# Kernel tuning notes

Measured on AMD Instinct MI355X. Metric: run time of the kernel, lower is better.

The kernel has to match this reference:

```python
import jax, jax.numpy as jnp
import numpy as np

HEADS, DIM_HEAD, LANDMARKS, PINV_ITERS = 8, 64, 256, 6
DIM, SIZE, N_CLASSES, N_PATCH = 512, 1024, 2, 16384
LN_EPS = 1e-5


def layer_norm(x, g, b):
    mu = x.mean(-1, keepdims=True)
    var = ((x - mu) ** 2).mean(-1, keepdims=True)
    return (x - mu) / jnp.sqrt(var + LN_EPS) * g + b


def moore_penrose_pinv(x, iters):
    # x: [b, h, m, m]; global max over all batch/head entries (matches torch.max)
    abs_x = jnp.abs(x)
    col = abs_x.sum(-1).max()
    row = abs_x.sum(-2).max()
    z = jnp.swapaxes(x, -1, -2) / (col * row)
    I = jnp.eye(x.shape[-1], dtype=x.dtype)
    for _ in range(iters):
        xz = x @ z
        z = 0.25 * z @ (13 * I - xz @ (15 * I - xz @ (7 * I - xz)))
    return z


def nystrom_attention(x, qkv_w, out_w, out_b, res_w):
    b, n, _ = x.shape
    m = LANDMARKS
    pad = (m - n % m) % m
    xp = jnp.pad(x, ((0, 0), (pad, 0), (0, 0)))  # pad at FRONT of sequence
    npad = n + pad
    qkv = xp @ qkv_w  # [b, npad, 3*h*d]
    q, k, v = jnp.split(qkv, 3, axis=-1)
    to_h = lambda t: t.reshape(b, npad, HEADS, DIM_HEAD).transpose(0, 2, 1, 3)
    q, k, v = to_h(q), to_h(k), to_h(v)
    q = q * (DIM_HEAD ** -0.5)
    l = npad // m  # tokens per landmark segment
    q_l = q.reshape(b, HEADS, m, l, DIM_HEAD).sum(3) / l
    k_l = k.reshape(b, HEADS, m, l, DIM_HEAD).sum(3) / l
    sim1 = jnp.einsum('bhid,bhjd->bhij', q, k_l)     # [b,h,npad,m]
    sim2 = jnp.einsum('bhid,bhjd->bhij', q_l, k_l)   # [b,h,m,m]
    sim3 = jnp.einsum('bhid,bhjd->bhij', q_l, k)     # [b,h,m,npad]
    a1 = jax.nn.softmax(sim1, -1)
    a2 = jax.nn.softmax(sim2, -1)
    a3 = jax.nn.softmax(sim3, -1)
    out = (a1 @ moore_penrose_pinv(a2, PINV_ITERS)) @ (a3 @ v)
    # residual depthwise conv over sequence dim, kernel (33,1), groups=heads
    res = jax.lax.conv_general_dilated(
        v, res_w, (1, 1), [(16, 16), (0, 0)],
        dimension_numbers=('NCHW', 'OIHW', 'NCHW'), feature_group_count=HEADS)
    out = out + res
    out = out.transpose(0, 2, 1, 3).reshape(b, npad, HEADS * DIM_HEAD)
    out = out @ out_w + out_b
    return out[:, -n:]


def trans_layer(x, ng, nb, qkv_w, out_w, out_b, res_w):
    return x + nystrom_attention(layer_norm(x, ng, nb), qkv_w, out_w, out_b, res_w)


def ppeg(x, w7, b7, w5, b5, w3, b3, H, W):
    cls_tok, feat = x[:, :1], x[:, 1:]
    B, N, C = feat.shape
    f = feat.transpose(0, 2, 1).reshape(B, C, H, W)
    def dw(w, b, p):
        y = jax.lax.conv_general_dilated(
            f, w, (1, 1), [(p, p), (p, p)],
            dimension_numbers=('NCHW', 'OIHW', 'NCHW'), feature_group_count=C)
        return y + b[None, :, None, None]
    out = dw(w7, b7, 3) + f + dw(w5, b5, 2) + dw(w3, b3, 1)
    out = out.reshape(B, C, H * W).transpose(0, 2, 1)
    return jnp.concatenate([cls_tok, out], axis=1)


def setup_inputs() -> dict:
    key = jax.random.key(0)
    ks = jax.random.split(key, 24)
    rn = lambda k, s, sc=0.02: jax.random.normal(k, s, jnp.float32) * sc
    inner = HEADS * DIM_HEAD  # 512
    return {
        'data': jax.random.normal(ks[0], (1, N_PATCH, SIZE), jnp.float32),
        'fc1_w': rn(ks[1], (SIZE, DIM)), 'fc1_b': jnp.zeros((DIM,), jnp.float32),
        'cls_token': jax.random.normal(ks[2], (1, 1, DIM), jnp.float32),
        'l1_ng': jnp.ones((DIM,), jnp.float32), 'l1_nb': jnp.zeros((DIM,), jnp.float32),
        'l1_qkv': rn(ks[3], (DIM, 3 * inner)),
        'l1_ow': rn(ks[4], (inner, DIM)), 'l1_ob': jnp.zeros((DIM,), jnp.float32),
        'l1_rw': rn(ks[5], (HEADS, 1, 33, 1)),
        'l2_ng': jnp.ones((DIM,), jnp.float32), 'l2_nb': jnp.zeros((DIM,), jnp.float32),
        'l2_qkv': rn(ks[6], (DIM, 3 * inner)),
        'l2_ow': rn(ks[7], (inner, DIM)), 'l2_ob': jnp.zeros((DIM,), jnp.float32),
        'l2_rw': rn(ks[8], (HEADS, 1, 33, 1)),
        'p_w7': rn(ks[9], (DIM, 1, 7, 7)), 'p_b7': jnp.zeros((DIM,), jnp.float32),
        'p_w5': rn(ks[10], (DIM, 1, 5, 5)), 'p_b5': jnp.zeros((DIM,), jnp.float32),
        'p_w3': rn(ks[11], (DIM, 1, 3, 3)), 'p_b3': jnp.zeros((DIM,), jnp.float32),
        'n_g': jnp.ones((DIM,), jnp.float32), 'n_b': jnp.zeros((DIM,), jnp.float32),
        'fc2_w': rn(ks[12], (DIM, N_CLASSES)), 'fc2_b': jnp.zeros((N_CLASSES,), jnp.float32),
    }


def reference(data, fc1_w, fc1_b, cls_token, l1_ng, l1_nb, l1_qkv, l1_ow, l1_ob, l1_rw,
              l2_ng, l2_nb, l2_qkv, l2_ow, l2_ob, l2_rw,
              p_w7, p_b7, p_w5, p_b5, p_w3, p_b3, n_g, n_b, fc2_w, fc2_b):
    h = jax.nn.relu(data @ fc1_w + fc1_b)  # [B, N, 512]
    B, N = h.shape[0], h.shape[1]
    _H = _W = int(np.ceil(np.sqrt(N)))
    add_length = _H * _W - N
    h = jnp.concatenate([h, h[:, :add_length, :]], axis=1)
    cls = jnp.broadcast_to(cls_token, (B, 1, h.shape[2]))
    h = jnp.concatenate([cls, h], axis=1)
    h = trans_layer(h, l1_ng, l1_nb, l1_qkv, l1_ow, l1_ob, l1_rw)
    h = ppeg(h, p_w7, p_b7, p_w5, p_b5, p_w3, p_b3, _H, _W)
    h = trans_layer(h, l2_ng, l2_nb, l2_qkv, l2_ow, l2_ob, l2_rw)
    h = layer_norm(h, n_g, n_b)[:, 0]
    logits = h @ fc2_w + fc2_b
    y_hat = jnp.argmax(logits, axis=1)
    y_prob = jax.nn.softmax(logits, axis=1)
    return (logits, y_prob, y_hat)
```

## Files before the change

### kernel.cpp

```cpp
#include <hip/hip_runtime.h>
#include <hip/hip_bf16.h>


#define NT 16385
#define NP 16640
#define PADR 255
#define DIMF 512
#define QKVW 1536
#define NHEAD 8
#define DH 64
#define NLM 256
#define LSEG 65
#define A3V_TC 20

typedef short bf16x8 __attribute__((ext_vector_type(8)));
typedef short bf16x4 __attribute__((ext_vector_type(4)));
typedef float f32x4 __attribute__((ext_vector_type(4)));

__device__ __forceinline__ void gload_lds16(const void* g, void* l) {
    __builtin_amdgcn_global_load_lds(
        (const __attribute__((address_space(1))) void*)g,
        (__attribute__((address_space(3))) void*)l, 16, 0, 0);
}

__device__ __forceinline__ float2 b2f(const __hip_bfloat16* p) {
    ushort2 u = *(const ushort2*)p;
    float2 r;
    r.x = __uint_as_float((unsigned)u.x << 16);
    r.y = __uint_as_float((unsigned)u.y << 16);
    return r;
}

__device__ __forceinline__ unsigned f2b16(float a, float b) {
    union { unsigned u; __hip_bfloat16 h[2]; } c;
    c.h[0] = __float2bfloat16(a); c.h[1] = __float2bfloat16(b);
    return c.u;
}

__device__ __forceinline__ bf16x4 f4b(float a, float b, float c, float d) {
    union { bf16x4 v; __hip_bfloat16 h[4]; } u;
    u.h[0] = __float2bfloat16(a); u.h[1] = __float2bfloat16(b);
    u.h[2] = __float2bfloat16(c); u.h[3] = __float2bfloat16(d);
    return u.v;
}

__global__ __launch_bounds__(256) void gemm_bf16_k(
    const __hip_bfloat16* __restrict__ A, const __hip_bfloat16* __restrict__ BT,
    const float* __restrict__ bias, const float* __restrict__ Cacc,
    float* __restrict__ C, __hip_bfloat16* __restrict__ C16,
    int M, int N, int K, int MA, int relu)
{
    __shared__ __align__(16) __hip_bfloat16 Asl[128 * 64];
    __shared__ __align__(16) __hip_bfloat16 Bsl[128 * 64];
    int tid = threadIdx.x;
    int wid = tid >> 6, lane = tid & 63;
    int m0 = blockIdx.y << 7, n0 = blockIdx.x << 7;
    int wr = (wid >> 1) << 6, wc = (wid & 1) << 6;
    f32x4 acc[4][4] = {};
    int lr = lane >> 3, lk = (lane & 7) << 3;
    for (int kt = 0; kt < K; kt += 64) {
#pragma unroll
        for (int i = 0; i < 4; ++i) {
            int ch = wid * 4 + i;
            int rowA = m0 + ch * 8 + lr;
            rowA = rowA < MA ? rowA : (MA - 1);
            gload_lds16(A + (size_t)rowA * K + kt + lk, &Asl[ch * 512]);
            int rowB = n0 + ch * 8 + lr;
            gload_lds16(BT + (size_t)rowB * K + kt + lk, &Bsl[ch * 512]);
        }
        __syncthreads();
#pragma unroll
        for (int ks = 0; ks < 2; ++ks) {
            int kb = ks * 32 + (lane >> 4) * 8;
            bf16x8 af[4], bfr[4];
#pragma unroll
            for (int m = 0; m < 4; ++m)
                af[m] = *(const bf16x8*)&Asl[(wr + m * 16 + (lane & 15)) * 64 + kb];
#pragma unroll
            for (int n = 0; n < 4; ++n)
                bfr[n] = *(const bf16x8*)&Bsl[(wc + n * 16 + (lane & 15)) * 64 + kb];
#pragma unroll
            for (int m = 0; m < 4; ++m)
#pragma unroll
                for (int n = 0; n < 4; ++n)
                    acc[m][n] = __builtin_amdgcn_mfma_f32_16x16x32_bf16(
                        af[m], bfr[n], acc[m][n], 0, 0, 0);
        }
        __syncthreads();
    }
    int cr = (lane >> 4) << 2, cc = lane & 15;
#pragma unroll
    for (int m = 0; m < 4; ++m) {
#pragma unroll
        for (int i = 0; i < 4; ++i) {
            int gm = m0 + wr + m * 16 + cr + i;
            if (gm >= M) continue;
#pragma unroll
            for (int n = 0; n < 4; ++n) {
                int gn = n0 + wc + n * 16 + cc;
                float v = acc[m][n][i];
                if (bias) v += bias[gn];
                if (Cacc) v += Cacc[(size_t)gm * N + gn];
                if (relu) v = fmaxf(v, 0.f);
                if (C16) C16[(size_t)gm * N + gn] = __float2bfloat16(v);
                else C[(size_t)gm * N + gn] = v;
            }
        }
    }
}

__global__ __launch_bounds__(256) void transcvt_k(const float* __restrict__ W,
    __hip_bfloat16* __restrict__ WT, int K, int N)
{
    __shared__ float t[32][33];
    int nt = N >> 5;
    int n0 = (blockIdx.x % nt) << 5, k0 = (blockIdx.x / nt) << 5;
    int tx = threadIdx.x & 31, ty = threadIdx.x >> 5;
    for (int r = ty; r < 32; r += 8) t[r][tx] = W[(size_t)(k0 + r) * N + n0 + tx];
    __syncthreads();
    for (int r = ty; r < 32; r += 8)
        WT[(size_t)(n0 + r) * K + k0 + tx] = __float2bfloat16(t[tx][r]);
}

__global__ __launch_bounds__(256) void cvt_k(const float4* __restrict__ in,
    ushort4* __restrict__ out, int n4)
{
    int i = blockIdx.x * 256 + threadIdx.x;
    if (i >= n4) return;
    float4 v = in[i];
    union { __hip_bfloat16 h[4]; ushort4 u; } cv;
    cv.h[0] = __float2bfloat16(v.x); cv.h[1] = __float2bfloat16(v.y);
    cv.h[2] = __float2bfloat16(v.z); cv.h[3] = __float2bfloat16(v.w);
    out[i] = cv.u;
}

__global__ __launch_bounds__(256) void vtrans_k(const __hip_bfloat16* __restrict__ qkvb16,
    __hip_bfloat16* __restrict__ vT16)
{
    int h = blockIdx.y;
    int t0 = blockIdx.x << 6;
    __shared__ float tile[64][65];
    int tid = threadIdx.x;
    for (int e = tid; e < 512; e += 256) {
        int r = e >> 3, c8 = (e & 7) << 3;
        union { bf16x8 v; __hip_bfloat16 hh[8]; } u;
        u.v = *(const bf16x8*)(qkvb16 + (size_t)(t0 + r) * QKVW + 1024 + (h << 6) + c8);
#pragma unroll
        for (int j = 0; j < 8; ++j) tile[r][c8 + j] = __bfloat162float(u.hh[j]);
    }
    __syncthreads();
    for (int e = tid; e < 512; e += 256) {
        int d = e >> 3, t8 = (e & 7) << 3;
        union { bf16x8 v; __hip_bfloat16 hh[8]; } u;
#pragma unroll
        for (int j = 0; j < 8; ++j) u.hh[j] = __float2bfloat16(tile[t8 + j][d]);
        *(bf16x8*)(vT16 + ((size_t)(h << 6) + d) * NP + t0 + t8) = u.v;
    }
}

__global__ __launch_bounds__(64) void ln_k(const float* __restrict__ in,
    const float* __restrict__ g, const float* __restrict__ b,
    __hip_bfloat16* __restrict__ out, int rows)
{
    int r = blockIdx.x;
    if (r >= rows) return;
    int lane = threadIdx.x;
    const float* xr = in + (size_t)r * DIMF;
    float v[8], s = 0.f;
#pragma unroll
    for (int i = 0; i < 8; ++i) { v[i] = xr[i * 64 + lane]; s += v[i]; }
#pragma unroll
    for (int off = 32; off; off >>= 1) s += __shfl_xor(s, off);
    float mu = s * (1.f / 512.f);
    float vs = 0.f;
#pragma unroll
    for (int i = 0; i < 8; ++i) { float d = v[i] - mu; vs += d * d; }
#pragma unroll
    for (int off = 32; off; off >>= 1) vs += __shfl_xor(vs, off);
    float rstd = rsqrtf(vs * (1.f / 512.f) + 1e-5f);
    __hip_bfloat16* orow = out + (size_t)r * DIMF;
#pragma unroll
    for (int i = 0; i < 8; ++i) {
        int d = i * 64 + lane;
        orow[d] = __float2bfloat16((v[i] - mu) * rstd * g[d] + b[d]);
    }
}

__global__ __launch_bounds__(256) void landmark_k(const __hip_bfloat16* __restrict__ qkvb16,
    float* __restrict__ ql, float* __restrict__ kl,
    __hip_bfloat16* __restrict__ ql16, __hip_bfloat16* __restrict__ kl16)
{
    int bx = blockIdx.x;
    int h = bx >> 8, j = bx & 255;
    int w = threadIdx.x >> 6, d = threadIdx.x & 63;
    __shared__ float pq[4][64], pk[4][64];
    float qs = 0.f, ks = 0.f;
    for (int u = w; u < LSEG; u += 4) {
        size_t addr = (size_t)(j * LSEG + u) * QKVW + (h << 6) + d;
        qs += __bfloat162float(qkvb16[addr]);
        ks += __bfloat162float(qkvb16[addr + 512]);
    }
    pq[w][d] = qs; pk[w][d] = ks;
    __syncthreads();
    if (threadIdx.x < 64) {
        float q = pq[0][d] + pq[1][d] + pq[2][d] + pq[3][d];
        float k = pk[0][d] + pk[1][d] + pk[2][d] + pk[3][d];
        float qm = q * (1.f / 65.f) * 0.125f;
        float km = k * (1.f / 65.f);
        ql[(size_t)bx * 64 + d] = qm;
        kl[(size_t)bx * 64 + d] = km;
        ql16[(size_t)bx * 64 + d] = __float2bfloat16(qm);
        kl16[(size_t)bx * 64 + d] = __float2bfloat16(km);
    }
}

__global__ __launch_bounds__(256) void a2_k(const float* __restrict__ ql,
    const float* __restrict__ kl, float* __restrict__ a2, __hip_bfloat16* __restrict__ a2_16)
{
    int h = blockIdx.x >> 8, i = blockIdx.x & 255;
    int j = threadIdx.x;
    __shared__ float qs[64];
    __shared__ float red[256];
    if (j < 64) qs[j] = ql[((size_t)(h << 8) + i) * 64 + j];
    __syncthreads();
    const float* kr = kl + ((size_t)(h << 8) + j) * 64;
    float s = 0.f;
#pragma unroll 8
    for (int d = 0; d < 64; ++d) s += qs[d] * kr[d];
    red[j] = s; __syncthreads();
    for (int st = 128; st; st >>= 1) { if (j < st) red[j] = fmaxf(red[j], red[j + st]); __syncthreads(); }
    float mx = red[0]; __syncthreads();
    float p = __expf(s - mx);
    red[j] = p; __syncthreads();
    for (int st = 128; st; st >>= 1) { if (j < st) red[j] += red[j + st]; __syncthreads(); }
    float v = p / red[0];
    a2[((size_t)h << 16) + i * 256 + j] = v;
    a2_16[((size_t)h << 16) + i * 256 + j] = __float2bfloat16(v);
}

__global__ __launch_bounds__(256) void zinit_k(const float* __restrict__ a2,
    __hip_bfloat16* __restrict__ zr16, __hip_bfloat16* __restrict__ zT16)
{
    int h = blockIdx.x, t = threadIdx.x;
    const float* X = a2 + ((size_t)h << 16);
    __shared__ float red[256];
    __shared__ float tl[64][65];
    float rs = 0.f;
    const float4* Xr = (const float4*)(X + (size_t)t * 256);
    for (int j = 0; j < 64; ++j) {
        float4 v = Xr[j];
        rs += fabsf(v.x) + fabsf(v.y) + fabsf(v.z) + fabsf(v.w);
    }
    red[t] = rs; __syncthreads();
    for (int st = 128; st; st >>= 1) { if (t < st) red[t] = fmaxf(red[t], red[t + st]); __syncthreads(); }
    float colv = red[0]; __syncthreads();
    float cs = 0.f;
    for (int i = 0; i < 256; ++i) cs += fabsf(X[i * 256 + t]);
    red[t] = cs; __syncthreads();
    for (int st = 128; st; st >>= 1) { if (t < st) red[t] = fmaxf(red[t], red[t + st]); __syncthreads(); }
    float rowv = red[0];
    float inv = 1.f / (colv * rowv);
    int cl = t & 63, rg = t >> 6;
    for (int tr = 0; tr < 4; ++tr)
        for (int tc = 0; tc < 4; ++tc) {
            __syncthreads();
#pragma unroll
            for (int k = 0; k < 16; ++k) {
                int rl = (k << 2) + rg;
                tl[rl][cl] = X[(size_t)(tr * 64 + rl) * 256 + tc * 64 + cl];
            }
            __syncthreads();
#pragma unroll
            for (int k = 0; k < 16; ++k) {
                int rl = (k << 2) + rg;
                zT16[((size_t)h << 16) + (size_t)(tr * 64 + rl) * 256 + tc * 64 + cl] =
                    __float2bfloat16(tl[rl][cl] * inv);
                zr16[((size_t)h << 16) + (size_t)(tc * 64 + rl) * 256 + tr * 64 + cl] =
                    __float2bfloat16(tl[cl][rl] * inv);
            }
        }
}

__global__ __launch_bounds__(256) void pgemm1_k(
    const __hip_bfloat16* __restrict__ a2_16, const __hip_bfloat16* __restrict__ zT16,
    __hip_bfloat16* __restrict__ xz16, __hip_bfloat16* __restrict__ t1T16)
{
    int h = blockIdx.y, n0 = blockIdx.x << 6;
    int lane = threadIdx.x & 63;
    int r0 = (threadIdx.x >> 6) << 6;
    int rA = lane & 15, g = lane >> 4, kp = g << 3;
    const __hip_bfloat16* Ah = a2_16 + ((size_t)h << 16);
    const __hip_bfloat16* Bh = zT16 + ((size_t)h << 16);
    f32x4 acc[4][4] = {};
    for (int ks = 0; ks < 8; ++ks) {
        bf16x8 af[4], bfr[4];
#pragma unroll
        for (int m = 0; m < 4; ++m)
            af[m] = *(const bf16x8*)&Ah[(size_t)(r0 + m * 16 + rA) * 256 + ks * 32 + kp];
#pragma unroll
        for (int n = 0; n < 4; ++n)
            bfr[n] = *(const bf16x8*)&Bh[(size_t)(n0 + n * 16 + rA) * 256 + ks * 32 + kp];
#pragma unroll
        for (int m = 0; m < 4; ++m)
#pragma unroll
            for (int n = 0; n < 4; ++n)
                acc[m][n] = __builtin_amdgcn_mfma_f32_16x16x32_bf16(af[m], bfr[n], acc[m][n], 0, 0, 0);
    }
    __hip_bfloat16* xzh = xz16 + ((size_t)h << 16);
    __hip_bfloat16* t1h = t1T16 + ((size_t)h << 16);
#pragma unroll
    for (int m = 0; m < 4; ++m)
#pragma unroll
        for (int i = 0; i < 4; ++i) {
            int gr = r0 + m * 16 + (g << 2) + i;
#pragma unroll
            for (int n = 0; n < 4; ++n) {
                int gc = n0 + n * 16 + rA;
                float v = acc[m][n][i];
                xzh[(size_t)gr * 256 + gc] = __float2bfloat16(v);
                t1h[(size_t)gc * 256 + gr] = __float2bfloat16((gr == gc ? 7.f : 0.f) - v);
            }
        }
}

__global__ __launch_bounds__(256) void pgemm3_k(
    const __hip_bfloat16* __restrict__ xz16, const __hip_bfloat16* __restrict__ t1T16,
    const __hip_bfloat16* __restrict__ zr16,
    __hip_bfloat16* __restrict__ znr16, __hip_bfloat16* __restrict__ znT16)
{
    __shared__ __align__(16) __hip_bfloat16 tA[64][264];
    __shared__ __align__(16) __hip_bfloat16 tB[64][264];
    int h = blockIdx.y, n0 = blockIdx.x << 6;
    int lane = threadIdx.x & 63;
    int r0 = (threadIdx.x >> 6) << 6;
    int rA = lane & 15, g = lane >> 4, kp = g << 3;
    const __hip_bfloat16* Xh = xz16 + ((size_t)h << 16);
    const __hip_bfloat16* T1h = t1T16 + ((size_t)h << 16);
    {
        f32x4 acc[4][4] = {};
        for (int ks = 0; ks < 8; ++ks) {
            bf16x8 af[4], bfr[4];
#pragma unroll
            for (int m = 0; m < 4; ++m)
                af[m] = *(const bf16x8*)&Xh[(size_t)(r0 + m * 16 + rA) * 256 + ks * 32 + kp];
#pragma unroll
            for (int n = 0; n < 4; ++n)
                bfr[n] = *(const bf16x8*)&T1h[(size_t)(n0 + n * 16 + rA) * 256 + ks * 32 + kp];
#pragma unroll
            for (int m = 0; m < 4; ++m)
#pragma unroll
                for (int n = 0; n < 4; ++n)
                    acc[m][n] = __builtin_amdgcn_mfma_f32_16x16x32_bf16(af[m], bfr[n], acc[m][n], 0, 0, 0);
        }
#pragma unroll
        for (int m = 0; m < 4; ++m)
#pragma unroll
            for (int n = 0; n < 4; ++n) {
                int gr0 = r0 + m * 16 + (g << 2);
                int cl = n * 16 + rA;
                *(bf16x4*)&tA[cl][gr0] = f4b(
                    ((gr0 + 0 == n0 + cl) ? 15.f : 0.f) - acc[m][n][0],
                    ((gr0 + 1 == n0 + cl) ? 15.f : 0.f) - acc[m][n][1],
                    ((gr0 + 2 == n0 + cl) ? 15.f : 0.f) - acc[m][n][2],
                    ((gr0 + 3 == n0 + cl) ? 15.f : 0.f) - acc[m][n][3]);
            }
    }
    __syncthreads();
    {
        f32x4 acc[4][4] = {};
        for (int ks = 0; ks < 8; ++ks) {
            bf16x8 af[4], bfr[4];
#pragma unroll
            for (int m = 0; m < 4; ++m)
                af[m] = *(const bf16x8*)&Xh[(size_t)(r0 + m * 16 + rA) * 256 + ks * 32 + kp];
#pragma unroll
            for (int n = 0; n < 4; ++n)
                bfr[n] = *(const bf16x8*)&tA[n * 16 + rA][ks * 32 + kp];
#pragma unroll
            for (int m = 0; m < 4; ++m)
#pragma unroll
                for (int n = 0; n < 4; ++n)
                    acc[m][n] = __builtin_amdgcn_mfma_f32_16x16x32_bf16(af[m], bfr[n], acc[m][n], 0, 0, 0);
        }
#pragma unroll
        for (int m = 0; m < 4; ++m)
#pragma unroll
            for (int n = 0; n < 4; ++n) {
                int gr0 = r0 + m * 16 + (g << 2);
                int cl = n * 16 + rA;
                *(bf16x4*)&tB[cl][gr0] = f4b(
                    ((gr0 + 0 == n0 + cl) ? 13.f : 0.f) - acc[m][n][0],
                    ((gr0 + 1 == n0 + cl) ? 13.f : 0.f) - acc[m][n][1],
                    ((gr0 + 2 == n0 + cl) ? 13.f : 0.f) - acc[m][n][2],
                    ((gr0 + 3 == n0 + cl) ? 13.f : 0.f) - acc[m][n][3]);
            }
    }
    __syncthreads();
    {
        const __hip_bfloat16* Zh = zr16 + ((size_t)h << 16);
        f32x4 acc[4][4] = {};
        for (int ks = 0; ks < 8; ++ks) {
            bf16x8 af[4], bfr[4];
#pragma unroll
            for (int m = 0; m < 4; ++m)
                af[m] = *(const bf16x8*)&Zh[(size_t)(r0 + m * 16 + rA) * 256 + ks * 32 + kp];
#pragma unroll
            for (int n = 0; n < 4; ++n)
                bfr[n] = *(const bf16x8*)&tB[n * 16 + rA][ks * 32 + kp];
#pragma unroll
            for (int m = 0; m < 4; ++m)
#pragma unroll
                for (int n = 0; n < 4; ++n)
                    acc[m][n] = __builtin_amdgcn_mfma_f32_16x16x32_bf16(af[m], bfr[n], acc[m][n], 0, 0, 0);
        }
        __hip_bfloat16* zrh = znr16 + ((size_t)h << 16);
        __hip_bfloat16* zth = znT16 + ((size_t)h << 16);
#pragma unroll
        for (int m = 0; m < 4; ++m)
#pragma unroll
            for (int i = 0; i < 4; ++i) {
                int gr = r0 + m * 16 + (g << 2) + i;
#pragma unroll
                for (int n = 0; n < 4; ++n) {
                    int gc = n0 + n * 16 + rA;
                    float v = 0.25f * acc[m][n][i];
                    zrh[(size_t)gr * 256 + gc] = __float2bfloat16(v);
                    zth[(size_t)gc * 256 + gr] = __float2bfloat16(v);
                }
            }
    }
}

__global__ __launch_bounds__(256) void wm_k(
    const __hip_bfloat16* __restrict__ zr16, const __hip_bfloat16* __restrict__ a3vT16,
    __hip_bfloat16* __restrict__ wmT16)
{
    int h = blockIdx.x;
    int lane = threadIdx.x & 63;
    int r0 = (threadIdx.x >> 6) << 6;
    int rA = lane & 15, g = lane >> 4, kp = g << 3;
    const __hip_bfloat16* Zh = zr16 + ((size_t)h << 16);
    const __hip_bfloat16* Bh = a3vT16 + ((size_t)h << 14);
    f32x4 acc[4][4] = {};
    for (int ks = 0; ks < 8; ++ks) {
        bf16x8 af[4], bfr[4];
#pragma unroll
        for (int m = 0; m < 4; ++m)
            af[m] = *(const bf16x8*)&Zh[(size_t)(r0 + m * 16 + rA) * 256 + ks * 32 + kp];
#pragma unroll
        for (int n = 0; n < 4; ++n)
            bfr[n] = *(const bf16x8*)&Bh[(size_t)(n * 16 + rA) * 256 + ks * 32 + kp];
#pragma unroll
        for (int m = 0; m < 4; ++m)
#pragma unroll
            for (int n = 0; n < 4; ++n)
                acc[m][n] = __builtin_amdgcn_mfma_f32_16x16x32_bf16(af[m], bfr[n], acc[m][n], 0, 0, 0);
    }
    __hip_bfloat16* Wh = wmT16 + ((size_t)h << 14);
#pragma unroll
    for (int m = 0; m < 4; ++m)
#pragma unroll
        for (int i = 0; i < 4; ++i) {
            int gr = r0 + m * 16 + (g << 2) + i;
#pragma unroll
            for (int n = 0; n < 4; ++n)
                Wh[(size_t)(n * 16 + rA) * 256 + gr] = __float2bfloat16(acc[m][n][i]);
        }
}

__global__ __launch_bounds__(128) void a3v_flash_k(
    const __hip_bfloat16* __restrict__ ql16, const __hip_bfloat16* __restrict__ qkvb16,
    const __hip_bfloat16* __restrict__ vT16,
    float* __restrict__ opart, float* __restrict__ mpart, float* __restrict__ lpart)
{
    int bx = blockIdx.x;
    int h = bx >> 2, qb = bx & 3;
    int tc = blockIdx.y;
    int wv = threadIdx.x >> 6;
    int lane = threadIdx.x & 63;
    int rA = lane & 15, g = lane >> 4, kp = g << 3;
    __shared__ __align__(16) __hip_bfloat16 Plds[2][32 * 64];
    char* P = (char*)&Plds[wv][0];

    bf16x8 qa[2][2];
    const __hip_bfloat16* qlh = ql16 + ((size_t)h << 14);
#pragma unroll
    for (int m = 0; m < 2; ++m)
#pragma unroll
        for (int ks = 0; ks < 2; ++ks)
            qa[m][ks] = *(const bf16x8*)(qlh +
                (size_t)((qb << 6) + (wv << 5) + (m << 4) + rA) * 64 + ks * 32 + kp);

    const __hip_bfloat16* kg = qkvb16 + 512 + (h << 6);
    const __hip_bfloat16* vg = vT16 + ((size_t)(h << 6)) * NP;

    f32x4 O[2][4] = {};
    float m_[2][4], l_[2][4];
#pragma unroll
    for (int m = 0; m < 2; ++m)
#pragma unroll
        for (int i = 0; i < 4; ++i) { m_[m][i] = -3e38f; l_[m][i] = 0.f; }

    for (int tile = tc * 13; tile < tc * 13 + 13; ++tile) {
        int t0 = tile << 6;
        f32x4 S[2][4] = {};
#pragma unroll
        for (int n = 0; n < 4; ++n)
#pragma unroll
            for (int ks = 0; ks < 2; ++ks) {
                bf16x8 kb = *(const bf16x8*)(kg + (size_t)(t0 + (n << 4) + rA) * QKVW + ks * 32 + kp);
                S[0][n] = __builtin_amdgcn_mfma_f32_16x16x32_bf16(qa[0][ks], kb, S[0][n], 0, 0, 0);
                S[1][n] = __builtin_amdgcn_mfma_f32_16x16x32_bf16(qa[1][ks], kb, S[1][n], 0, 0, 0);
            }
        float f_[2][4];
#pragma unroll
        for (int m = 0; m < 2; ++m)
#pragma unroll
            for (int i = 0; i < 4; ++i) {
                float mx = fmaxf(fmaxf(S[m][0][i], S[m][1][i]), fmaxf(S[m][2][i], S[m][3][i]));
#pragma unroll
                for (int msk = 8; msk; msk >>= 1) mx = fmaxf(mx, __shfl_xor(mx, msk));
                float mn = fmaxf(m_[m][i], mx);
                float f = __expf(m_[m][i] - mn);
                int r = (m << 4) + (g << 2) + i;
                int swz = (r & 7) << 4;
                float sum = 0.f;
#pragma unroll
                for (int n = 0; n < 4; ++n) {
                    float p = __expf(S[m][n][i] - mn);
                    sum += p;
                    int byte = (r << 7) + (((n << 4) + rA) << 1);
                    *(__hip_bfloat16*)(P + (byte ^ swz)) = __float2bfloat16(p);
                }
#pragma unroll
                for (int msk = 8; msk; msk >>= 1) sum += __shfl_xor(sum, msk);
                l_[m][i] = l_[m][i] * f + sum;
                m_[m][i] = mn;
                f_[m][i] = f;
            }
#pragma unroll
        for (int m = 0; m < 2; ++m)
#pragma unroll
            for (int i = 0; i < 4; ++i) {
                float f = f_[m][i];
#pragma unroll
                for (int n = 0; n < 4; ++n) O[m][n][i] *= f;
            }
#pragma unroll
        for (int ks2 = 0; ks2 < 2; ++ks2) {
            bf16x8 pa[2];
#pragma unroll
            for (int m = 0; m < 2; ++m) {
                int rr = (m << 4) + rA;
                int byte = (rr << 7) + ((ks2 * 32 + kp) << 1);
                pa[m] = *(const bf16x8*)(P + (byte ^ ((rr & 7) << 4)));
            }
#pragma unroll
            for (int n = 0; n < 4; ++n) {
                bf16x8 vb = *(const bf16x8*)(vg + (size_t)((n << 4) + rA) * NP + t0 + ks2 * 32 + kp);
                O[0][n] = __builtin_amdgcn_mfma_f32_16x16x32_bf16(pa[0], vb, O[0][n], 0, 0, 0);
                O[1][n] = __builtin_amdgcn_mfma_f32_16x16x32_bf16(pa[1], vb, O[1][n], 0, 0, 0);
            }
        }
    }
    int pb2 = (bx << 1) | wv;
    size_t obase = ((size_t)pb2 * A3V_TC + tc) * 2048;
#pragma unroll
    for (int m = 0; m < 2; ++m)
#pragma unroll
        for (int i = 0; i < 4; ++i) {
            int r = (m << 4) + (g << 2) + i;
#pragma unroll
            for (int n = 0; n < 4; ++n)
                opart[obase + (size_t)r * 64 + (n << 4) + rA] = O[m][n][i];
            if (rA == 0) {
                mpart[((size_t)pb2 * A3V_TC + tc) * 32 + r] = m_[m][i];
                lpart[((size_t)pb2 * A3V_TC + tc) * 32 + r] = l_[m][i];
            }
        }
}

__global__ __launch_bounds__(64) void a3v_comb_k(const float* __restrict__ opart,
    const float* __restrict__ mpart, const float* __restrict__ lpart,
    __hip_bfloat16* __restrict__ a3vT16)
{
    int pb = blockIdx.x, d = threadIdx.x;
    int h = pb >> 3;
    for (int r = 0; r < 32; ++r) {
        float M = -3e38f;
        for (int tc = 0; tc < A3V_TC; ++tc)
            M = fmaxf(M, mpart[((size_t)pb * A3V_TC + tc) * 32 + r]);
        float L = 0.f, od = 0.f;
        for (int tc = 0; tc < A3V_TC; ++tc) {
            float w = __expf(mpart[((size_t)pb * A3V_TC + tc) * 32 + r] - M);
            L += lpart[((size_t)pb * A3V_TC + tc) * 32 + r] * w;
            od += w * opart[((size_t)pb * A3V_TC + tc) * 2048 + (size_t)r * 64 + d];
        }
        int j = ((pb & 7) << 5) + r;
        a3vT16[((size_t)((h << 6) + d) << 8) + j] = __float2bfloat16(od / L);
    }
}

__global__ __launch_bounds__(128) void attnout_mfma_k(
    const __hip_bfloat16* __restrict__ qkvb16, const __hip_bfloat16* __restrict__ kl16,
    const __hip_bfloat16* __restrict__ wmT16, float* __restrict__ o)
{
    int h = blockIdx.y;
    int rbase = (blockIdx.x << 6) + ((threadIdx.x >> 6) << 5);
    int lane = threadIdx.x & 63;
    int rA = lane & 15;
    int g = lane >> 4;
    int kp = g << 3;
    __shared__ __align__(16) __hip_bfloat16 Plds[2][32 * 256];
    char* P = (char*)&Plds[threadIdx.x >> 6][0];

    bf16x8 qa[2][2];
#pragma unroll
    for (int m = 0; m < 2; ++m)
#pragma unroll
        for (int ks = 0; ks < 2; ++ks)
            qa[m][ks] = *(const bf16x8*)(qkvb16 +
                (size_t)(rbase + m * 16 + rA) * QKVW + (h << 6) + ks * 32 + kp);

    const __hip_bfloat16* klh = kl16 + ((size_t)h << 14);
    f32x4 S[2][16] = {};
#pragma unroll
    for (int n = 0; n < 16; ++n) {
#pragma unroll
        for (int ks = 0; ks < 2; ++ks) {
            bf16x8 kb = *(const bf16x8*)(klh + (size_t)((n << 4) + rA) * 64 + ks * 32 + kp);
            S[0][n] = __builtin_amdgcn_mfma_f32_16x16x32_bf16(qa[0][ks], kb, S[0][n], 0, 0, 0);
            S[1][n] = __builtin_amdgcn_mfma_f32_16x16x32_bf16(qa[1][ks], kb, S[1][n], 0, 0, 0);
        }
    }
#pragma unroll
    for (int m = 0; m < 2; ++m)
#pragma unroll
        for (int n = 0; n < 16; ++n) S[m][n] *= 0.125f;

    float lsum[2][4];
#pragma unroll
    for (int m = 0; m < 2; ++m)
#pragma unroll
        for (int i = 0; i < 4; ++i) {
            float mx = -3e38f;
#pragma unroll
            for (int n = 0; n < 16; ++n) mx = fmaxf(mx, S[m][n][i]);
#pragma unroll
            for (int msk = 8; msk; msk >>= 1) mx = fmaxf(mx, __shfl_xor(mx, msk));
            float sum = 0.f;
            int r = (m << 4) + (g << 2) + i;
            int swz = (r & 7) << 4;
#pragma unroll
            for (int n = 0; n < 16; ++n) {
                float p = __expf(S[m][n][i] - mx);
                sum += p;
                int byte = (r << 9) + (((n << 4) + rA) << 1);
                *(__hip_bfloat16*)(P + (byte ^ swz)) = __float2bfloat16(p);
            }
#pragma unroll
            for (int msk = 8; msk; msk >>= 1) sum += __shfl_xor(sum, msk);
            lsum[m][i] = sum;
        }

    const __hip_bfloat16* wmh = wmT16 + ((size_t)h << 14);
    f32x4 O[2][4] = {};
#pragma unroll
    for (int kc = 0; kc < 8; ++kc) {
        bf16x8 pa[2];
#pragma unroll
        for (int m = 0; m < 2; ++m) {
            int rr = (m << 4) + rA;
            int byte = (rr << 9) + (((kc << 5) + kp) << 1);
            pa[m] = *(const bf16x8*)(P + (byte ^ ((rr & 7) << 4)));
        }
#pragma unroll
        for (int n = 0; n < 4; ++n) {
            bf16x8 wb = *(const bf16x8*)(wmh + (size_t)((n << 4) + rA) * 256 + (kc << 5) + kp);
#pragma unroll
            for (int m = 0; m < 2; ++m)
                O[m][n] = __builtin_amdgcn_mfma_f32_16x16x32_bf16(pa[m], wb, O[m][n], 0, 0, 0);
        }
    }
#pragma unroll
    for (int m = 0; m < 2; ++m)
#pragma unroll
        for (int i = 0; i < 4; ++i) {
            float inv = 1.f / lsum[m][i];
            int gm = rbase + (m << 4) + (g << 2) + i;
#pragma unroll
            for (int n = 0; n < 4; ++n)
                o[(size_t)gm * DIMF + (h << 6) + (n << 4) + rA] = O[m][n][i] * inv;
        }
}

__global__ __launch_bounds__(256) void resconv_tile_k(const __hip_bfloat16* __restrict__ qkvb16,
    const float* __restrict__ rw, const float* __restrict__ oin,
    __hip_bfloat16* __restrict__ oout)
{
    int cg = blockIdx.y;
    int t0 = blockIdx.x << 7;
    int tid = threadIdx.x;
    int lane = tid & 63, w = tid >> 6;
    __shared__ float vt[160][64];
    __shared__ float wr[33];
    if (tid < 33) wr[tid] = rw[cg * 33 + tid];
    for (int e = tid; e < 160 * 64; e += 256) {
        int tt = e >> 6, l = e & 63;
        int t = t0 - 16 + tt;
        vt[tt][l] = (t >= 0 && t < NP)
            ? __bfloat162float(qkvb16[(size_t)t * QKVW + 1024 + (cg << 6) + l]) : 0.f;
    }
    __syncthreads();
    for (int i = 0; i < 32; ++i) {
        int tl = (w << 5) + i;
        float acc = 0.f;
#pragma unroll
        for (int ky = 0; ky < 33; ++ky) acc += wr[ky] * vt[tl + ky][lane];
        size_t oi = (size_t)(t0 + tl) * DIMF + (cg << 6) + lane;
        oout[oi] = __float2bfloat16(oin[oi] + acc);
    }
}

__global__ __launch_bounds__(256) void ppeg3_k(const float* __restrict__ x,
    const float* __restrict__ w7, const float* __restrict__ b7,
    const float* __restrict__ w5, const float* __restrict__ b5,
    const float* __restrict__ w3, const float* __restrict__ b3,
    float* __restrict__ outfeat)
{
    int cg = blockIdx.y;
    int ty0 = (blockIdx.x >> 4) << 3, tx0 = (blockIdx.x & 15) << 3;
    int tid = threadIdx.x;
    int cgi = tid & 15;
    int xo = (tid >> 4) & 7;
    int yb0 = (tid >> 7) << 2;
    int c = (cg << 5) + (cgi << 1);
    const float* feat = x + DIMF;
    __shared__ __align__(16) __hip_bfloat16 tile[196][32];
    __shared__ __align__(16) __hip_bfloat16 ws7[49][32];
    __shared__ __align__(16) __hip_bfloat16 ws5[25][32];
    __shared__ __align__(16) __hip_bfloat16 ws3[9][32];
    for (int e = tid; e < 49 * 32; e += 256) {
        int t = e >> 5, cl = e & 31;
        ws7[t][cl] = __float2bfloat16(w7[(size_t)((cg << 5) + cl) * 49 + t]);
    }
    for (int e = tid; e < 25 * 32; e += 256) {
        int t = e >> 5, cl = e & 31;
        ws5[t][cl] = __float2bfloat16(w5[(size_t)((cg << 5) + cl) * 25 + t]);
    }
    for (int e = tid; e < 9 * 32; e += 256) {
        int t = e >> 5, cl = e & 31;
        ws3[t][cl] = __float2bfloat16(w3[(size_t)((cg << 5) + cl) * 9 + t]);
    }
    for (int e = tid; e < 196 * 16; e += 256) {
        int sp = e >> 4, cp = (e & 15) << 1;
        int yy = ty0 - 3 + sp / 14, xc = tx0 - 3 + sp % 14;
        float2 v = make_float2(0.f, 0.f);
        if ((unsigned)yy < 128u && (unsigned)xc < 128u)
            v = *(const float2*)&feat[(size_t)(yy * 128 + xc) * DIMF + (cg << 5) + cp];
        *(unsigned*)&tile[sp][cp] = f2b16(v.x, v.y);
    }
    __syncthreads();
    float2 bs7 = *(const float2*)&b7[c], bs5 = *(const float2*)&b5[c], bs3 = *(const float2*)&b3[c];
    float bsx = bs7.x + bs5.x + bs3.x, bsy = bs7.y + bs5.y + bs3.y;
    float2 acc[4];
#pragma unroll
    for (int o = 0; o < 4; ++o) {
        float2 idv = *(const float2*)&feat[(size_t)((ty0 + yb0 + o) * 128 + tx0 + xo) * DIMF + c];
        acc[o].x = idv.x + bsx;
        acc[o].y = idv.y + bsy;
    }
    int c2 = cgi << 1;
#pragma unroll
    for (int kx = 0; kx < 7; ++kx) {
        float2 wc[7];
#pragma unroll
        for (int j = 0; j < 7; ++j) wc[j] = b2f(&ws7[j * 7 + kx][c2]);
#pragma unroll
        for (int r = 0; r < 10; ++r) {
            float2 v = b2f(&tile[(yb0 + r) * 14 + xo + kx][c2]);
#pragma unroll
            for (int o = 0; o < 4; ++o) {
                int ky = r - o;
                if (ky >= 0 && ky < 7) {
                    acc[o].x += wc[ky].x * v.x; acc[o].y += wc[ky].y * v.y;
                }
            }
        }
    }
#pragma unroll
    for (int kx = 0; kx < 5; ++kx) {
        float2 wc[5];
#pragma unroll
        for (int j = 0; j < 5; ++j) wc[j] = b2f(&ws5[j * 5 + kx][c2]);
#pragma unroll
        for (int r = 0; r < 8; ++r) {
            float2 v = b2f(&tile[(yb0 + 1 + r) * 14 + xo + 1 + kx][c2]);
#pragma unroll
            for (int o = 0; o < 4; ++o) {
                int ky = r - o;
                if (ky >= 0 && ky < 5) {
                    acc[o].x += wc[ky].x * v.x; acc[o].y += wc[ky].y * v.y;
                }
            }
        }
    }
#pragma unroll
    for (int kx = 0; kx < 3; ++kx) {
        float2 wc[3];
#pragma unroll
        for (int j = 0; j < 3; ++j) wc[j] = b2f(&ws3[j * 3 + kx][c2]);
#pragma unroll
        for (int r = 0; r < 6; ++r) {
            float2 v = b2f(&tile[(yb0 + 2 + r) * 14 + xo + 2 + kx][c2]);
#pragma unroll
            for (int o = 0; o < 4; ++o) {
                int ky = r - o;
                if (ky >= 0 && ky < 3) {
                    acc[o].x += wc[ky].x * v.x; acc[o].y += wc[ky].y * v.y;
                }
            }
        }
    }
#pragma unroll
    for (int o = 0; o < 4; ++o)
        *(float2*)&outfeat[(size_t)((ty0 + yb0 + o) * 128 + tx0 + xo) * DIMF + c] = acc[o];
}

__global__ __launch_bounds__(64) void head_k(const float* __restrict__ x,
    const float* __restrict__ g, const float* __restrict__ b,
    const float* __restrict__ w, const float* __restrict__ bias, float* __restrict__ out)
{
    int lane = threadIdx.x;
    float v[8], s = 0.f;
#pragma unroll
    for (int i = 0; i < 8; ++i) { v[i] = x[i * 64 + lane]; s += v[i]; }
#pragma unroll
    for (int off = 32; off; off >>= 1) s += __shfl_xor(s, off);
    float mu = s * (1.f / 512.f);
    float vs = 0.f;
#pragma unroll
    for (int i = 0; i < 8; ++i) { float d = v[i] - mu; vs += d * d; }
#pragma unroll
    for (int off = 32; off; off >>= 1) vs += __shfl_xor(vs, off);
    float rstd = rsqrtf(vs * (1.f / 512.f) + 1e-5f);
    float l0 = 0.f, l1 = 0.f;
#pragma unroll
    for (int i = 0; i < 8; ++i) {
        int d = i * 64 + lane;
        float hn = (v[i] - mu) * rstd * g[d] + b[d];
        l0 += hn * w[d * 2];
        l1 += hn * w[d * 2 + 1];
    }
#pragma unroll
    for (int off = 32; off; off >>= 1) { l0 += __shfl_xor(l0, off); l1 += __shfl_xor(l1, off); }
    if (lane == 0) {
        l0 += bias[0]; l1 += bias[1];
        float m = fmaxf(l0, l1);
        float e0 = __expf(l0 - m), e1 = __expf(l1 - m);
        float ss = e0 + e1;
        out[0] = l0; out[1] = l1;
        out[2] = e0 / ss; out[3] = e1 / ss;
        out[4] = (l1 > l0) ? 1.f : 0.f;
    }
}

extern "C" void kernel_launch(void* const* d_in, const int* in_sizes, int n_in,
                              void* d_out, int out_size, void* d_ws, size_t ws_size,
                              hipStream_t stream)
{
    (void)in_sizes; (void)n_in; (void)out_size; (void)ws_size;
    const float* data   = (const float*)d_in[0];
    const float* fc1_w  = (const float*)d_in[1];
    const float* fc1_b  = (const float*)d_in[2];
    const float* cls    = (const float*)d_in[3];
    const float* l1_ng  = (const float*)d_in[4];
    const float* l1_nb  = (const float*)d_in[5];
    const float* l1_qkv = (const float*)d_in[6];
    const float* l1_ow  = (const float*)d_in[7];
    const float* l1_ob  = (const float*)d_in[8];
    const float* l1_rw  = (const float*)d_in[9];
    const float* l2_ng  = (const float*)d_in[10];
    const float* l2_nb  = (const float*)d_in[11];
    const float* l2_qkv = (const float*)d_in[12];
    const float* l2_ow  = (const float*)d_in[13];
    const float* l2_ob  = (const float*)d_in[14];
    const float* l2_rw  = (const float*)d_in[15];
    const float* p_w7   = (const float*)d_in[16];
    const float* p_b7   = (const float*)d_in[17];
    const float* p_w5   = (const float*)d_in[18];
    const float* p_b5   = (const float*)d_in[19];
    const float* p_w3   = (const float*)d_in[20];
    const float* p_b3   = (const float*)d_in[21];
    const float* n_g    = (const float*)d_in[22];
    const float* n_b    = (const float*)d_in[23];
    const float* fc2_w  = (const float*)d_in[24];
    const float* fc2_b  = (const float*)d_in[25];

    char* base = (char*)d_ws;
    auto carve = [&](size_t bytes) { char* p = base; base += (bytes + 255) & ~(size_t)255; return p; };
    float* x               = (float*)carve((size_t)NT * DIMF * 4);
    float* x2              = (float*)carve((size_t)NT * DIMF * 4);
    __hip_bfloat16* xp16   = (__hip_bfloat16*)carve((size_t)NP * DIMF * 2);
    __hip_bfloat16* qkvb16 = (__hip_bfloat16*)carve((size_t)NP * QKVW * 2);
    __hip_bfloat16* vT16   = (__hip_bfloat16*)carve((size_t)NHEAD * DH * NP * 2);
    float* obuf            = (float*)carve((size_t)NP * DIMF * 4);
    __hip_bfloat16* wT     = (__hip_bfloat16*)carve((size_t)QKVW * DIMF * 2);
    float* ql              = (float*)carve(131072 * 4);
    float* kl              = (float*)carve(131072 * 4);
    __hip_bfloat16* ql16   = (__hip_bfloat16*)carve(131072 * 2);
    __hip_bfloat16* kl16   = (__hip_bfloat16*)carve(131072 * 2);
    __hip_bfloat16* wmT16  = (__hip_bfloat16*)carve(131072 * 2);
    float* a2              = (float*)carve(524288 * 4);
    __hip_bfloat16* a2_16  = (__hip_bfloat16*)carve(524288 * 2);
    __hip_bfloat16* zrA    = (__hip_bfloat16*)carve(524288 * 2);
    __hip_bfloat16* zrB    = (__hip_bfloat16*)carve(524288 * 2);
    __hip_bfloat16* ztA    = (__hip_bfloat16*)carve(524288 * 2);
    __hip_bfloat16* ztB    = (__hip_bfloat16*)carve(524288 * 2);
    __hip_bfloat16* xz16   = (__hip_bfloat16*)carve(524288 * 2);
    __hip_bfloat16* t1T16  = (__hip_bfloat16*)carve(524288 * 2);
    __hip_bfloat16* a3vT16 = (__hip_bfloat16*)carve(131072 * 2);
    float* opart = (float*)carve((size_t)64 * A3V_TC * 2048 * 4);
    float* mpart = (float*)carve((size_t)64 * A3V_TC * 32 * 4);
    float* lpart = (float*)carve((size_t)64 * A3V_TC * 32 * 4);
    __hip_bfloat16* obuf2  = xp16;
    __hip_bfloat16* data16 = qkvb16;

    cvt_k<<<(16384 * 1024 / 4 + 255) / 256, 256, 0, stream>>>(
        (const float4*)data, (ushort4*)data16, 16384 * 1024 / 4);
    transcvt_k<<<(DIMF / 32) * (1024 / 32), 256, 0, stream>>>(fc1_w, wT, 1024, DIMF);
    gemm_bf16_k<<<dim3(DIMF / 128, 16384 / 128), 256, 0, stream>>>(
        data16, wT, fc1_b, nullptr, x + DIMF, nullptr, 16384, DIMF, 1024, 16384, 1);
    hipMemcpyAsync(x, cls, DIMF * sizeof(float), hipMemcpyDeviceToDevice, stream);

    auto layer = [&](float* xv, const float* ng, const float* nb, const float* qw,
                     const float* ow, const float* ob, const float* rw) {
        hipMemsetAsync(xp16, 0, (size_t)PADR * DIMF * 2, stream);
        ln_k<<<NT, 64, 0, stream>>>(xv, ng, nb, xp16 + (size_t)PADR * DIMF, NT);
        transcvt_k<<<(QKVW / 32) * (DIMF / 32), 256, 0, stream>>>(qw, wT, DIMF, QKVW);
        gemm_bf16_k<<<dim3(QKVW / 128, NP / 128), 256, 0, stream>>>(
            xp16, wT, nullptr, nullptr, nullptr, qkvb16, NP, QKVW, DIMF, NP, 0);
        vtrans_k<<<dim3(NP / 64, NHEAD), 256, 0, stream>>>(qkvb16, vT16);
        landmark_k<<<NHEAD * NLM, 256, 0, stream>>>(qkvb16, ql, kl, ql16, kl16);
        a2_k<<<NHEAD * NLM, 256, 0, stream>>>(ql, kl, a2, a2_16);
        zinit_k<<<NHEAD, 256, 0, stream>>>(a2, zrA, ztA);
        __hip_bfloat16 *zr = zrA, *zt = ztA, *zrN = zrB, *ztN = ztB;
        for (int it = 0; it < 6; ++it) {
            pgemm1_k<<<dim3(4, NHEAD), 256, 0, stream>>>(a2_16, zt, xz16, t1T16);
            pgemm3_k<<<dim3(4, NHEAD), 256, 0, stream>>>(xz16, t1T16, zr, zrN, ztN);
            __hip_bfloat16* t;
            t = zr; zr = zrN; zrN = t;
            t = zt; zt = ztN; ztN = t;
        }
        a3v_flash_k<<<dim3(32, A3V_TC), 128, 0, stream>>>(ql16, qkvb16, vT16, opart, mpart, lpart);
        a3v_comb_k<<<64, 64, 0, stream>>>(opart, mpart, lpart, a3vT16);
        wm_k<<<NHEAD, 256, 0, stream>>>(zr, a3vT16, wmT16);
        attnout_mfma_k<<<dim3(NP / 64, NHEAD), 128, 0, stream>>>(qkvb16, kl16, wmT16, obuf);
        resconv_tile_k<<<dim3(NP / 128, NHEAD), 256, 0, stream>>>(qkvb16, rw, obuf, obuf2);
        transcvt_k<<<(DIMF / 32) * (DIMF / 32), 256, 0, stream>>>(ow, wT, DIMF, DIMF);
        gemm_bf16_k<<<dim3(DIMF / 128, (NT + 127) / 128), 256, 0, stream>>>(
            obuf2 + (size_t)PADR * DIMF, wT, ob, xv, xv, nullptr, NT, DIMF, DIMF, NT, 0);
    };

    layer(x, l1_ng, l1_nb, l1_qkv, l1_ow, l1_ob, l1_rw);

    ppeg3_k<<<dim3(256, 16), 256, 0, stream>>>(x, p_w7, p_b7, p_w5, p_b5, p_w3, p_b3, x2 + DIMF);
    hipMemcpyAsync(x2, x, DIMF * sizeof(float), hipMemcpyDeviceToDevice, stream);

    layer(x2, l2_ng, l2_nb, l2_qkv, l2_ow, l2_ob, l2_rw);

    head_k<<<1, 64, 0, stream>>>(x2, n_g, n_b, fc2_w, fc2_b, (float*)d_out);
}
```

Before: 1.344 ms.

## Double-buffer GEMM LDS, remap workgroups across XCDs, store attention output in bf16

The bf16 GEMM now double-buffers its LDS tiles, issuing the next K-tile's global-to-LDS loads before computing on the current tile. It also remaps block indices so each XCD gets a contiguous range of output tiles, aiming for better L2 locality. Separately, the attention output buffer between attnout and resconv is stored as bf16 instead of fp32, halving that round-trip traffic at some precision cost. Double buffering doubles LDS use per block (64KB), which may reduce occupancy.

```diff
diff --git a/kernel.cpp b/kernel.cpp
--- a/kernel.cpp
+++ b/kernel.cpp
@@ -50,35 +50,46 @@
     float* __restrict__ C, __hip_bfloat16* __restrict__ C16,
     int M, int N, int K, int MA, int relu)
 {
-    __shared__ __align__(16) __hip_bfloat16 Asl[128 * 64];
-    __shared__ __align__(16) __hip_bfloat16 Bsl[128 * 64];
+    __shared__ __align__(16) __hip_bfloat16 Asl[2][128 * 64];
+    __shared__ __align__(16) __hip_bfloat16 Bsl[2][128 * 64];
     int tid = threadIdx.x;
     int wid = tid >> 6, lane = tid & 63;
-    int m0 = blockIdx.y << 7, n0 = blockIdx.x << 7;
+    int nwg = (int)(gridDim.x * gridDim.y);
+    int orig = (int)(blockIdx.y * gridDim.x + blockIdx.x);
+    int qq = nwg >> 3, rr = nwg & 7;
+    int xcd = orig & 7, idx = orig >> 3;
+    int wg = (xcd < rr ? xcd * (qq + 1) : rr * (qq + 1) + (xcd - rr) * qq) + idx;
+    int m0 = (wg / (int)gridDim.x) << 7, n0 = (wg % (int)gridDim.x) << 7;
     int wr = (wid >> 1) << 6, wc = (wid & 1) << 6;
     f32x4 acc[4][4] = {};
     int lr = lane >> 3, lk = (lane & 7) << 3;
-    for (int kt = 0; kt < K; kt += 64) {
+    int nt = K >> 6;
+    auto stage = [&](int buf, int kt) {
 #pragma unroll
         for (int i = 0; i < 4; ++i) {
             int ch = wid * 4 + i;
             int rowA = m0 + ch * 8 + lr;
             rowA = rowA < MA ? rowA : (MA - 1);
-            gload_lds16(A + (size_t)rowA * K + kt + lk, &Asl[ch * 512]);
+            gload_lds16(A + (size_t)rowA * K + kt + lk, &Asl[buf][ch * 512]);
             int rowB = n0 + ch * 8 + lr;
-            gload_lds16(BT + (size_t)rowB * K + kt + lk, &Bsl[ch * 512]);
-        }
-        __syncthreads();
+            gload_lds16(BT + (size_t)rowB * K + kt + lk, &Bsl[buf][ch * 512]);
+        }
+    };
+    stage(0, 0);
+    __syncthreads();
+    int cur = 0;
+    for (int t = 0; t < nt; ++t) {
+        if (t + 1 < nt) stage(cur ^ 1, (t + 1) << 6);
 #pragma unroll
         for (int ks = 0; ks < 2; ++ks) {
             int kb = ks * 32 + (lane >> 4) * 8;
             bf16x8 af[4], bfr[4];
 #pragma unroll
             for (int m = 0; m < 4; ++m)
-                af[m] = *(const bf16x8*)&Asl[(wr + m * 16 + (lane & 15)) * 64 + kb];
+                af[m] = *(const bf16x8*)&Asl[cur][(wr + m * 16 + (lane & 15)) * 64 + kb];
 #pragma unroll
             for (int n = 0; n < 4; ++n)
-                bfr[n] = *(const bf16x8*)&Bsl[(wc + n * 16 + (lane & 15)) * 64 + kb];
+                bfr[n] = *(const bf16x8*)&Bsl[cur][(wc + n * 16 + (lane & 15)) * 64 + kb];
 #pragma unroll
             for (int m = 0; m < 4; ++m)
 #pragma unroll
@@ -87,6 +98,7 @@
                         af[m], bfr[n], acc[m][n], 0, 0, 0);
         }
         __syncthreads();
+        cur ^= 1;
     }
     int cr = (lane >> 4) << 2, cc = lane & 15;
 #pragma unroll
@@ -603,7 +615,7 @@
 
 __global__ __launch_bounds__(128) void attnout_mfma_k(
     const __hip_bfloat16* __restrict__ qkvb16, const __hip_bfloat16* __restrict__ kl16,
-    const __hip_bfloat16* __restrict__ wmT16, float* __restrict__ o)
+    const __hip_bfloat16* __restrict__ wmT16, __hip_bfloat16* __restrict__ o)
 {
     int h = blockIdx.y;
     int rbase = (blockIdx.x << 6) + ((threadIdx.x >> 6) << 5);
@@ -690,12 +702,13 @@
             int gm = rbase + (m << 4) + (g << 2) + i;
 #pragma unroll
             for (int n = 0; n < 4; ++n)
-                o[(size_t)gm * DIMF + (h << 6) + (n << 4) + rA] = O[m][n][i] * inv;
+                o[(size_t)gm * DIMF + (h << 6) + (n << 4) + rA] =
+                    __float2bfloat16(O[m][n][i] * inv);
         }
 }
 
 __global__ __launch_bounds__(256) void resconv_tile_k(const __hip_bfloat16* __restrict__ qkvb16,
-    const float* __restrict__ rw, const float* __restrict__ oin,
+    const float* __restrict__ rw, const __hip_bfloat16* __restrict__ oin,
     __hip_bfloat16* __restrict__ oout)
 {
     int cg = blockIdx.y;
@@ -718,7 +731,7 @@
 #pragma unroll
         for (int ky = 0; ky < 33; ++ky) acc += wr[ky] * vt[tl + ky][lane];
         size_t oi = (size_t)(t0 + tl) * DIMF + (cg << 6) + lane;
-        oout[oi] = __float2bfloat16(oin[oi] + acc);
+        oout[oi] = __float2bfloat16(__bfloat162float(oin[oi]) + acc);
     }
 }
 
@@ -904,6 +917,7 @@
     __hip_bfloat16* xp16   = (__hip_bfloat16*)carve((size_t)NP * DIMF * 2);
     __hip_bfloat16* qkvb16 = (__hip_bfloat16*)carve((size_t)NP * QKVW * 2);
     __hip_bfloat16* vT16   = (__hip_bfloat16*)carve((size_t)NHEAD * DH * NP * 2);
+    __hip_bfloat16* obuf16 = (__hip_bfloat16*)carve((size_t)NP * DIMF * 2);
     float* obuf            = (float*)carve((size_t)NP * DIMF * 4);
     __hip_bfloat16* wT     = (__hip_bfloat16*)carve((size_t)QKVW * DIMF * 2);
     float* ql              = (float*)carve(131072 * 4);
@@ -955,8 +969,8 @@
         a3v_flash_k<<<dim3(32, A3V_TC), 128, 0, stream>>>(ql16, qkvb16, vT16, opart, mpart, lpart);
         a3v_comb_k<<<64, 64, 0, stream>>>(opart, mpart, lpart, a3vT16);
         wm_k<<<NHEAD, 256, 0, stream>>>(zr, a3vT16, wmT16);
-        attnout_mfma_k<<<dim3(NP / 64, NHEAD), 128, 0, stream>>>(qkvb16, kl16, wmT16, obuf);
-        resconv_tile_k<<<dim3(NP / 128, NHEAD), 256, 0, stream>>>(qkvb16, rw, obuf, obuf2);
+        attnout_mfma_k<<<dim3(NP / 64, NHEAD), 128, 0, stream>>>(qkvb16, kl16, wmT16, obuf16);
+        resconv_tile_k<<<dim3(NP / 128, NHEAD), 256, 0, stream>>>(qkvb16, rw, obuf16, obuf2);
         transcvt_k<<<(DIMF / 32) * (DIMF / 32), 256, 0, stream>>>(ow, wT, DIMF, DIMF);
         gemm_bf16_k<<<dim3(DIMF / 128, (NT + 127) / 128), 256, 0, stream>>>(
             obuf2 + (size_t)PADR * DIMF, wT, ob, xv, xv, nullptr, NT, DIMF, DIMF, NT, 0);
```

Measured after the change: 1.410 ms. 4.9% more time.
